# Performance work log

Hardware: AMD Instinct MI355X
Metric: run time of the kernel (lower is better)

The kernel has to match this reference:

```python
import jax, jax.numpy as jnp
import numpy as np

B, S, D = 1, 8192, 768
T_MAX = 1000.0  # timestamp range (days); keeps beta*tau <= 1 so exp is well-behaved


def setup_inputs() -> dict:
    key = jax.random.key(0)
    k1, k2 = jax.random.split(key)
    h = jax.random.normal(k1, (B, S, D), dtype=jnp.float32)
    # timestamps: sorted ascending per timeline (posts arrive in time order)
    t = jnp.sort(jax.random.uniform(k2, (B, S), dtype=jnp.float32) * T_MAX, axis=-1)
    # learned scalar parameters of HeatLayer
    epsilon = jnp.asarray(0.01, dtype=jnp.float32)
    beta = jnp.asarray(0.001, dtype=jnp.float32)
    return {"h": h, "t": t, "epsilon": epsilon, "beta": beta}


def reference(h, t, epsilon, beta):
    """HEAT layer: out[b,i] = sum_{j: t[i]>=t[j]} h[b,j] + relu(h[b,j]) * eps * exp(beta*(t[i]-t[j])).

    Matches apply_heat_on_matrix_representations with temporal_direction='past',
    exclude_current_post=False, sum_decay_with_original=True,
    allow_negative_decay=False, background_intensity='default', no padding.
    """
    tau = t[:, :, None] - t[:, None, :]            # [B,S,S] pairwise time deltas
    mask = (tau >= 0).astype(h.dtype)              # causal (past incl. current) mask
    W = epsilon * jnp.exp(beta * tau) * mask       # Hawkes decay weights
    out = jnp.einsum('bij,bjd->bid', mask, h) \
        + jnp.einsum('bij,bjd->bid', W, jnp.maximum(h, 0.0))
    return out
```

## Files before the change

kernel.cpp:

```cpp
#include <hip/hip_runtime.h>


namespace {
constexpr int S   = 8192;
constexpr int D   = 768;
constexpr int DV  = D / 4;
constexpr int CH  = 32;
constexpr int NC  = S / CH;
constexpr int QL  = 64;
constexpr int NG  = DV / QL;
constexpr int RG  = 4;
constexpr int RR  = CH / RG;
constexpr int SEG = 16;
constexpr int CPS = NC / SEG;
constexpr int QPB = 16;
constexpr int SBP = DV / QPB;
}

__device__ __forceinline__ float4 f4add(float4 a, float4 b) {
    return make_float4(a.x + b.x, a.y + b.y, a.z + b.z, a.w + b.w);
}
__device__ __forceinline__ void f4relu_fma(float4& acc, float4 h, float d) {
    acc.x += fmaxf(h.x, 0.f) * d;
    acc.y += fmaxf(h.y, 0.f) * d;
    acc.z += fmaxf(h.z, 0.f) * d;
    acc.w += fmaxf(h.w, 0.f) * d;
}

__global__ __launch_bounds__(256)
void heat_partials(const float* __restrict__ h, const float* __restrict__ t,
                   const float* __restrict__ betap,
                   float4* __restrict__ SP, float4* __restrict__ SQ) {
    const int tid = threadIdx.x, lane = tid & (QL - 1), r = tid >> 6;
    const int c = blockIdx.x, g = blockIdx.y;
    const int q = g * QL + lane;
    __shared__ float dec[CH];
    __shared__ float4 rgP[RG][QL], rgQ[RG][QL];
    if (tid < CH) dec[tid] = expf(-betap[0] * t[c * CH + tid]);
    __syncthreads();
    const float4* h4 = (const float4*)h;
    const int row0 = c * CH + r * RR;
    float4 hv[RR];
#pragma unroll
    for (int k = 0; k < RR; ++k) hv[k] = h4[(size_t)(row0 + k) * DV + q];
    float4 pp = {0, 0, 0, 0}, qq = {0, 0, 0, 0};
#pragma unroll
    for (int k = 0; k < RR; ++k) {
        pp = f4add(pp, hv[k]);
        f4relu_fma(qq, hv[k], dec[r * RR + k]);
    }
    rgP[r][lane] = pp;
    rgQ[r][lane] = qq;
    __syncthreads();
    if (r == 0) {
        SP[c * DV + q] = f4add(f4add(rgP[0][lane], rgP[1][lane]),
                               f4add(rgP[2][lane], rgP[3][lane]));
        SQ[c * DV + q] = f4add(f4add(rgQ[0][lane], rgQ[1][lane]),
                               f4add(rgQ[2][lane], rgQ[3][lane]));
    }
}

__global__ __launch_bounds__(256)
void heat_scan(const float4* __restrict__ SP, const float4* __restrict__ SQ,
               float4* __restrict__ offP, float4* __restrict__ offQ) {
    const int blk = blockIdx.x;
    const bool isQ = blk >= SBP;
    const int lb = isQ ? blk - SBP : blk;
    const float4* src = isQ ? SQ : SP;
    float4*       dst = isQ ? offQ : offP;
    const int qk = threadIdx.x & (QPB - 1);
    const int sg = threadIdx.x >> 4;
    const int qs = lb * QPB + qk;
    const int c0 = sg * CPS;
    __shared__ float4 ssum[SEG][QPB];
    float4 v[CPS];
#pragma unroll
    for (int u = 0; u < CPS; ++u) v[u] = src[(c0 + u) * DV + qs];
    float4 tot = {0, 0, 0, 0};
#pragma unroll
    for (int u = 0; u < CPS; ++u) tot = f4add(tot, v[u]);
    ssum[sg][qk] = tot;
    __syncthreads();
    float4 run = {0, 0, 0, 0};
    for (int s2 = 0; s2 < SEG - 1; ++s2)
        if (s2 < sg) run = f4add(run, ssum[s2][qk]);
#pragma unroll
    for (int u = 0; u < CPS; ++u) {
        dst[(c0 + u) * DV + qs] = run;
        run = f4add(run, v[u]);
    }
}

__global__ __launch_bounds__(256)
void heat_out(const float* __restrict__ h, const float* __restrict__ t,
              const float* __restrict__ epsp, const float* __restrict__ betap,
              const float4* __restrict__ offP, const float4* __restrict__ offQ,
              float* __restrict__ out) {
    const int tid = threadIdx.x, lane = tid & (QL - 1), r = tid >> 6;
    const int c = blockIdx.x, g = blockIdx.y;
    const int q = g * QL + lane;
    const float eps = epsp[0], beta = betap[0];
    __shared__ float tt[CH + 1];
    __shared__ float4 rgP[RG][QL], rgQ[RG][QL];
    if (tid <= CH) {
        int j = c * CH + tid;
        tt[tid] = (j < S) ? t[j] : 1e30f;
    }
    __syncthreads();
    const float4* h4 = (const float4*)h;
    float4* out4 = (float4*)out;
    const int row0 = c * CH + r * RR;
    float4 hv[RR];
#pragma unroll
    for (int k = 0; k < RR; ++k) hv[k] = h4[(size_t)(row0 + k) * DV + q];
    float tv[RR], dc[RR];
#pragma unroll
    for (int k = 0; k < RR; ++k) {
        tv[k] = tt[r * RR + k];
        dc[k] = expf(-beta * tv[k]);
    }
    float4 pp = {0, 0, 0, 0}, qq = {0, 0, 0, 0};
#pragma unroll
    for (int k = 0; k < RR; ++k) {
        pp = f4add(pp, hv[k]);
        f4relu_fma(qq, hv[k], dc[k]);
    }
    rgP[r][lane] = pp;
    rgQ[r][lane] = qq;
    __syncthreads();
    float4 po = offP[c * DV + q];
    float4 qo = offQ[c * DV + q];
#pragma unroll
    for (int rr = 0; rr < RG - 1; ++rr)
        if (rr < r) {
            po = f4add(po, rgP[rr][lane]);
            qo = f4add(qo, rgQ[rr][lane]);
        }
#pragma unroll
    for (int k = 0; k < RR; ++k) {
        po = f4add(po, hv[k]);
        f4relu_fma(qo, hv[k], dc[k]);
        const float ep = eps * expf(beta * tv[k]);
        float4 o;
        o.x = po.x + ep * qo.x;
        o.y = po.y + ep * qo.y;
        o.z = po.z + ep * qo.z;
        o.w = po.w + ep * qo.w;
        const int lr = r * RR + k;
        if (tt[lr + 1] == tv[k]) {
            int j = row0 + k + 1;
            float tj = tt[lr + 1];
            while (tj == tv[k]) {
                float4 hj = h4[(size_t)j * DV + q];
                o.x += hj.x + eps * fmaxf(hj.x, 0.f);
                o.y += hj.y + eps * fmaxf(hj.y, 0.f);
                o.z += hj.z + eps * fmaxf(hj.z, 0.f);
                o.w += hj.w + eps * fmaxf(hj.w, 0.f);
                ++j;
                if (j >= S) break;
                const int lj = j - c * CH;
                tj = (lj <= CH) ? tt[lj] : t[j];
            }
        }
        out4[(size_t)(row0 + k) * DV + q] = o;
    }
}

extern "C" void kernel_launch(void* const* d_in, const int* in_sizes, int n_in,
                              void* d_out, int out_size, void* d_ws, size_t ws_size,
                              hipStream_t stream) {
    const float* h    = (const float*)d_in[0];
    const float* t    = (const float*)d_in[1];
    const float* eps  = (const float*)d_in[2];
    const float* beta = (const float*)d_in[3];
    float* out = (float*)d_out;

    float4* SP   = (float4*)d_ws;
    float4* SQ   = SP + NC * DV;
    float4* offP = SQ + NC * DV;
    float4* offQ = offP + NC * DV;

    heat_partials<<<dim3(NC, NG), 256, 0, stream>>>(h, t, beta, SP, SQ);
    heat_scan<<<2 * SBP, 256, 0, stream>>>(SP, SQ, offP, offQ);
    heat_out<<<dim3(NC, NG), 256, 0, stream>>>(h, t, eps, beta, offP, offQ, out);
}
```

Before: 21.46 us.

## Double chunk size, hoist loads before barriers, precompute decay tables, nontemporal stores

```diff
diff --git a/kernel.cpp b/kernel.cpp
--- a/kernel.cpp
+++ b/kernel.cpp
@@ -5,7 +5,7 @@
 constexpr int S   = 8192;
 constexpr int D   = 768;
 constexpr int DV  = D / 4;
-constexpr int CH  = 32;
+constexpr int CH  = 64;
 constexpr int NC  = S / CH;
 constexpr int QL  = 64;
 constexpr int NG  = DV / QL;
@@ -17,6 +17,8 @@
 constexpr int SBP = DV / QPB;
 }
 
+typedef float f4raw __attribute__((ext_vector_type(4)));
+
 __device__ __forceinline__ float4 f4add(float4 a, float4 b) {
     return make_float4(a.x + b.x, a.y + b.y, a.z + b.z, a.w + b.w);
 }
@@ -30,19 +32,19 @@
 __global__ __launch_bounds__(256)
 void heat_partials(const float* __restrict__ h, const float* __restrict__ t,
                    const float* __restrict__ betap,
-                   float4* __restrict__ SP, float4* __restrict__ SQ) {
+                   float4* __restrict__ SP1, float4* __restrict__ SQ1) {
     const int tid = threadIdx.x, lane = tid & (QL - 1), r = tid >> 6;
     const int c = blockIdx.x, g = blockIdx.y;
     const int q = g * QL + lane;
     __shared__ float dec[CH];
     __shared__ float4 rgP[RG][QL], rgQ[RG][QL];
-    if (tid < CH) dec[tid] = expf(-betap[0] * t[c * CH + tid]);
-    __syncthreads();
     const float4* h4 = (const float4*)h;
     const int row0 = c * CH + r * RR;
     float4 hv[RR];
 #pragma unroll
     for (int k = 0; k < RR; ++k) hv[k] = h4[(size_t)(row0 + k) * DV + q];
+    if (tid < CH) dec[tid] = expf(-betap[0] * t[c * CH + tid]);
+    __syncthreads();
     float4 pp = {0, 0, 0, 0}, qq = {0, 0, 0, 0};
 #pragma unroll
     for (int k = 0; k < RR; ++k) {
@@ -52,21 +54,21 @@
     rgP[r][lane] = pp;
     rgQ[r][lane] = qq;
     __syncthreads();
-    if (r == 0) {
-        SP[c * DV + q] = f4add(f4add(rgP[0][lane], rgP[1][lane]),
-                               f4add(rgP[2][lane], rgP[3][lane]));
-        SQ[c * DV + q] = f4add(f4add(rgQ[0][lane], rgQ[1][lane]),
-                               f4add(rgQ[2][lane], rgQ[3][lane]));
-    }
+    if (r == 0)
+        SP1[c * DV + q] = f4add(f4add(rgP[0][lane], rgP[1][lane]),
+                                f4add(rgP[2][lane], rgP[3][lane]));
+    else if (r == 1)
+        SQ1[c * DV + q] = f4add(f4add(rgQ[0][lane], rgQ[1][lane]),
+                                f4add(rgQ[2][lane], rgQ[3][lane]));
 }
 
 __global__ __launch_bounds__(256)
-void heat_scan(const float4* __restrict__ SP, const float4* __restrict__ SQ,
+void heat_scan(const float4* __restrict__ SP1, const float4* __restrict__ SQ1,
                float4* __restrict__ offP, float4* __restrict__ offQ) {
     const int blk = blockIdx.x;
     const bool isQ = blk >= SBP;
     const int lb = isQ ? blk - SBP : blk;
-    const float4* src = isQ ? SQ : SP;
+    const float4* src = isQ ? SQ1 : SP1;
     float4*       dst = isQ ? offQ : offP;
     const int qk = threadIdx.x & (QPB - 1);
     const int sg = threadIdx.x >> 4;
@@ -96,61 +98,74 @@
               const float* __restrict__ epsp, const float* __restrict__ betap,
               const float4* __restrict__ offP, const float4* __restrict__ offQ,
               float* __restrict__ out) {
-    const int tid = threadIdx.x, lane = tid & (QL - 1), r = tid >> 6;
-    const int c = blockIdx.x, g = blockIdx.y;
-    const int q = g * QL + lane;
+    const int tid  = threadIdx.x;
+    const int lane = tid & (QL - 1);
+    const int r    = tid >> 6;
+    const int c    = blockIdx.x;
+    const int g    = blockIdx.y;
+    const int q    = g * QL + lane;
     const float eps = epsp[0], beta = betap[0];
+
     __shared__ float tt[CH + 1];
+    __shared__ float dec[CH], epv[CH];
     __shared__ float4 rgP[RG][QL], rgQ[RG][QL];
+
+    const float4* h4   = (const float4*)h;
+    float4*       out4 = (float4*)out;
+    const int row0 = c * CH + r * RR;
+
+    float4 hv[RR];
+#pragma unroll
+    for (int k = 0; k < RR; ++k) hv[k] = h4[(size_t)(row0 + k) * DV + q];
+    float4 po = offP[(size_t)c * DV + q];
+    float4 qo = offQ[(size_t)c * DV + q];
+
     if (tid <= CH) {
         int j = c * CH + tid;
         tt[tid] = (j < S) ? t[j] : 1e30f;
     }
     __syncthreads();
-    const float4* h4 = (const float4*)h;
-    float4* out4 = (float4*)out;
-    const int row0 = c * CH + r * RR;
-    float4 hv[RR];
-#pragma unroll
-    for (int k = 0; k < RR; ++k) hv[k] = h4[(size_t)(row0 + k) * DV + q];
-    float tv[RR], dc[RR];
-#pragma unroll
-    for (int k = 0; k < RR; ++k) {
-        tv[k] = tt[r * RR + k];
-        dc[k] = expf(-beta * tv[k]);
-    }
-    float4 pp = {0, 0, 0, 0}, qq = {0, 0, 0, 0};
+    if (tid < CH) {
+        float tv = tt[tid];
+        dec[tid] = expf(-beta * tv);
+        epv[tid] = eps * expf(beta * tv);
+    }
+    __syncthreads();
+
+    const float4 z = {0, 0, 0, 0};
+    float4 pp = z, qq = z;
 #pragma unroll
     for (int k = 0; k < RR; ++k) {
         pp = f4add(pp, hv[k]);
-        f4relu_fma(qq, hv[k], dc[k]);
+        f4relu_fma(qq, hv[k], dec[r * RR + k]);
     }
     rgP[r][lane] = pp;
     rgQ[r][lane] = qq;
     __syncthreads();
-    float4 po = offP[c * DV + q];
-    float4 qo = offQ[c * DV + q];
-#pragma unroll
-    for (int rr = 0; rr < RG - 1; ++rr)
-        if (rr < r) {
-            po = f4add(po, rgP[rr][lane]);
-            qo = f4add(qo, rgQ[rr][lane]);
+
+#pragma unroll
+    for (int rr2 = 0; rr2 < RG - 1; ++rr2)
+        if (rr2 < r) {
+            po = f4add(po, rgP[rr2][lane]);
+            qo = f4add(qo, rgQ[rr2][lane]);
         }
+
 #pragma unroll
     for (int k = 0; k < RR; ++k) {
         po = f4add(po, hv[k]);
-        f4relu_fma(qo, hv[k], dc[k]);
-        const float ep = eps * expf(beta * tv[k]);
+        f4relu_fma(qo, hv[k], dec[r * RR + k]);
+        const float ep = epv[r * RR + k];
         float4 o;
         o.x = po.x + ep * qo.x;
         o.y = po.y + ep * qo.y;
         o.z = po.z + ep * qo.z;
         o.w = po.w + ep * qo.w;
         const int lr = r * RR + k;
-        if (tt[lr + 1] == tv[k]) {
+        if (tt[lr + 1] == tt[lr]) {
             int j = row0 + k + 1;
+            const float tcur = tt[lr];
             float tj = tt[lr + 1];
-            while (tj == tv[k]) {
+            while (tj == tcur) {
                 float4 hj = h4[(size_t)j * DV + q];
                 o.x += hj.x + eps * fmaxf(hj.x, 0.f);
                 o.y += hj.y + eps * fmaxf(hj.y, 0.f);
@@ -162,7 +177,8 @@
                 tj = (lj <= CH) ? tt[lj] : t[j];
             }
         }
-        out4[(size_t)(row0 + k) * DV + q] = o;
+        __builtin_nontemporal_store(*(const f4raw*)&o,
+            (f4raw*)(out4 + (size_t)(row0 + k) * DV + q));
     }
 }
 
@@ -175,12 +191,12 @@
     const float* beta = (const float*)d_in[3];
     float* out = (float*)d_out;
 
-    float4* SP   = (float4*)d_ws;
-    float4* SQ   = SP + NC * DV;
-    float4* offP = SQ + NC * DV;
-    float4* offQ = offP + NC * DV;
-
-    heat_partials<<<dim3(NC, NG), 256, 0, stream>>>(h, t, beta, SP, SQ);
-    heat_scan<<<2 * SBP, 256, 0, stream>>>(SP, SQ, offP, offQ);
+    float4* SP1  = (float4*)d_ws;
+    float4* SQ1  = SP1 + (size_t)NC * DV;
+    float4* offP = SQ1 + (size_t)NC * DV;
+    float4* offQ = offP + (size_t)NC * DV;
+
+    heat_partials<<<dim3(NC, NG), 256, 0, stream>>>(h, t, beta, SP1, SQ1);
+    heat_scan<<<2 * SBP, 256, 0, stream>>>(SP1, SQ1, offP, offQ);
     heat_out<<<dim3(NC, NG), 256, 0, stream>>>(h, t, eps, beta, offP, offQ, out);
 }
```

New measurement: 19.88 us. 1.08x faster.
